# Optimization experiments

Measured on AMD Instinct MI355X. Metric: run time of the kernel, lower is better.

## Reference

```python
import jax, jax.numpy as jnp
import numpy as np
import math

NEG = -100000.0

def sliding_window_attention(q, k, v, window_size, padding_mask):
    # q,k,v: [B,H,L,D]; padding_mask: [B,L] (0 = pad)
    B, H, L, D = q.shape
    w = window_size // 2
    W = 2 * w + 1
    kp = jnp.pad(k, ((0, 0), (0, 0), (w, w), (0, 0)))
    vp = jnp.pad(v, ((0, 0), (0, 0), (w, w), (0, 0)))
    # window gather indices in padded coordinates: position i attends padded [i, i+2w]
    idx = jnp.arange(L)[:, None] + jnp.arange(W)[None, :]        # [L,W]
    pos = idx - w                                                 # true key positions
    valid = (pos >= 0) & (pos < L)                                # [L,W]
    k_win = kp[:, :, idx]                                         # [B,H,L,W,D]
    scores = jnp.einsum('bhld,bhlwd->bhlw', q, k_win)             # [B,H,L,W]
    scores = jnp.where(valid[None, None], scores, NEG)
    if padding_mask is not None:
        neigh_ok = padding_mask[:, jnp.clip(pos, 0, L - 1)]       # [B,L,W]
        scores = jnp.where(neigh_ok[:, None] == 0, NEG, scores)
    attn = jax.nn.softmax(scores / math.sqrt(D), axis=-1)         # [B,H,L,W]
    v_win = vp[:, :, idx]                                         # [B,H,L,W,D]
    values = jnp.einsum('bhlw,bhlwd->bhld', attn, v_win)
    return values

def setup_inputs() -> dict:
    key = jax.random.key(0)
    ks = jax.random.split(key, 5)
    B, L, input_dim, E, H = 2, 2048, 1024, 1024, 16
    x = jax.random.normal(ks[0], (B, L, input_dim), dtype=jnp.float32)
    padding_mask = jnp.ones((B, L), dtype=jnp.int32)
    # xavier-uniform linear weights (torch Linear stores [out, in])
    lim_qkv = math.sqrt(6.0 / (input_dim + 3 * E))
    W_qkv = jax.random.uniform(ks[1], (3 * E, input_dim), minval=-lim_qkv, maxval=lim_qkv, dtype=jnp.float32)
    b_qkv = jnp.zeros((3 * E,), dtype=jnp.float32)
    lim_o = math.sqrt(6.0 / (E + E))
    W_o = jax.random.uniform(ks[2], (E, E), minval=-lim_o, maxval=lim_o, dtype=jnp.float32)
    b_o = jnp.zeros((E,), dtype=jnp.float32)
    return {"x": x, "padding_mask": padding_mask, "W_qkv": W_qkv, "b_qkv": b_qkv, "W_o": W_o, "b_o": b_o}

def reference(x, padding_mask, W_qkv, b_qkv, W_o, b_o):
    B, L, _ = x.shape
    E = W_o.shape[0]
    H = 16
    hd = E // H
    window_size = 64
    qkv = x @ W_qkv.T + b_qkv                                  # [B,L,3E]
    qkv = qkv.reshape(B, L, H, 3 * hd).transpose(0, 2, 1, 3)   # [B,H,L,3hd]
    q, k, v = jnp.split(qkv, 3, axis=-1)
    values = sliding_window_attention(q, k, v, window_size, padding_mask)
    values = values.transpose(0, 2, 1, 3).reshape(B, L, E)
    o = values @ W_o.T + b_o
    return o
```

## Files before the change

### kernel.cpp

```cpp
#include <hip/hip_runtime.h>
#include <hip/hip_bf16.h>

typedef unsigned int u32;
typedef unsigned short u16;
typedef __attribute__((ext_vector_type(8))) short short8;
typedef __attribute__((ext_vector_type(4))) float f32x4;

#define NEG_SCORE (-100000.0f)

__device__ __forceinline__ float bflo(u32 u) { return __uint_as_float(u << 16); }
__device__ __forceinline__ float bfhi(u32 u) { return __uint_as_float(u & 0xffff0000u); }
__device__ __forceinline__ u16 f2bf(float f) {
    u32 u = __float_as_uint(f);
    u32 r = (u + 0x7fffu + ((u >> 16) & 1u)) >> 16;
    return (u16)r;
}

__device__ __forceinline__ void async16(const u16* g, u16* l) {
    __builtin_amdgcn_global_load_lds(
        (const __attribute__((address_space(1))) u32*)g,
        (__attribute__((address_space(3))) u32*)l,
        16, 0, 0);
}

__global__ __launch_bounds__(256) void f32_to_bf16_kernel(
    const float* __restrict__ src, u16* __restrict__ dst)
{
    const int i = blockIdx.x * 256 + threadIdx.x;
    const float4* s4 = (const float4*)src;
    float4 a = s4[2 * i + 0];
    float4 b = s4[2 * i + 1];
    uint4 o;
    o.x = (u32)f2bf(a.x) | ((u32)f2bf(a.y) << 16);
    o.y = (u32)f2bf(a.z) | ((u32)f2bf(a.w) << 16);
    o.z = (u32)f2bf(b.x) | ((u32)f2bf(b.y) << 16);
    o.w = (u32)f2bf(b.z) | ((u32)f2bf(b.w) << 16);
    ((uint4*)dst)[i] = o;
}

template <bool OUT_BF16>
__global__ __launch_bounds__(256) void gemm_bt_bias(
    const u16* __restrict__ A, const u16* __restrict__ Bt,
    const float* __restrict__ bias, void* __restrict__ Cv,
    int M, int N, int K)
{
    __shared__ u16 sA[128 * 32];
    __shared__ u16 sB[128 * 32];

    const int t    = threadIdx.x;
    const int m0   = blockIdx.y * 128;
    const int n0   = blockIdx.x * 128;
    const int lane = t & 63;
    const int wv   = t >> 6;
    const int wm   = (wv & 1) * 64;
    const int wn   = (wv >> 1) * 64;
    const int lr   = lane & 15;
    const int quad = lane >> 4;

    const u16* pa = A  + (size_t)(m0 + (t >> 2)) * K + ((t & 3) << 3);
    const u16* pb = Bt + (size_t)(n0 + (t >> 2)) * K + ((t & 3) << 3);
    u16* la = &sA[t * 8];
    u16* lb = &sB[t * 8];
    const size_t half = (size_t)64 * K;

    const f32x4 zero4 = {0.f, 0.f, 0.f, 0.f};
    f32x4 acc[4][4];
#pragma unroll
    for (int mt = 0; mt < 4; mt++)
#pragma unroll
        for (int nt = 0; nt < 4; nt++) acc[mt][nt] = zero4;

    for (int kk = 0; kk < K; kk += 32) {
        async16(pa + kk, la);
        async16(pa + kk + half, la + 2048);
        async16(pb + kk, lb);
        async16(pb + kk + half, lb + 2048);
        __syncthreads();

        short8 af[4], bfr[4];
#pragma unroll
        for (int mt = 0; mt < 4; mt++)
            af[mt] = *(const short8*)&sA[(wm + mt * 16 + lr) * 32 + quad * 8];
#pragma unroll
        for (int nt = 0; nt < 4; nt++)
            bfr[nt] = *(const short8*)&sB[(wn + nt * 16 + lr) * 32 + quad * 8];

#pragma unroll
        for (int mt = 0; mt < 4; mt++)
#pragma unroll
            for (int nt = 0; nt < 4; nt++)
                acc[mt][nt] = __builtin_amdgcn_mfma_f32_16x16x32_bf16(
                    af[mt], bfr[nt], acc[mt][nt], 0, 0, 0);
        __syncthreads();
    }

    float bv[4];
#pragma unroll
    for (int nt = 0; nt < 4; nt++)
        bv[nt] = bias[n0 + wn + nt * 16 + lr];

#pragma unroll
    for (int mt = 0; mt < 4; mt++) {
#pragma unroll
        for (int i = 0; i < 4; i++) {
            size_t row = (size_t)(m0 + wm + mt * 16 + quad * 4 + i);
#pragma unroll
            for (int nt = 0; nt < 4; nt++) {
                float v = acc[mt][nt][i] + bv[nt];
                size_t idx = row * N + n0 + wn + nt * 16 + lr;
                if (OUT_BF16) ((u16*)Cv)[idx] = f2bf(v);
                else          ((float*)Cv)[idx] = v;
            }
        }
    }
}

#define ATT_L 2048
#define ATT_C3 3072

__global__ __launch_bounds__(256) void swa_kernel(
    const u16* __restrict__ qkv, const int* __restrict__ mask,
    u16* __restrict__ values)
{
    __shared__ u16 sQ[4096];
    __shared__ u16 sK[8192];
    __shared__ u16 sP[8192];
    __shared__ u16 sV[9728];
    __shared__ int smask[128];
    __shared__ float sInv[64];

    const int t  = threadIdx.x;
    const int q0 = blockIdx.x * 64;
    const int h  = blockIdx.y;
    const int b  = blockIdx.z;
    const size_t base_bl = (size_t)b * ATT_L;
    const int* mrow = mask + b * ATT_L;
    const u16* hbase = qkv + base_bl * ATT_C3 + h * 192;

#pragma unroll
    for (int rep = 0; rep < 2; rep++) {
        int u = t + rep * 256;
        int r = u >> 3, j = u & 7;
        uint4 d = *(const uint4*)(hbase + (size_t)(q0 + r) * ATT_C3 + j * 8);
        *(uint4*)&sQ[(j >> 2) * 2048 + r * 32 + (j & 3) * 8] = d;
    }
#pragma unroll
    for (int rep = 0; rep < 4; rep++) {
        int u = t + rep * 256;
        int r = u >> 3, j = u & 7;
        int pos = q0 - 32 + r;
        int pc = min(max(pos, 0), ATT_L - 1);
        uint4 d = *(const uint4*)(hbase + (size_t)pc * ATT_C3 + 64 + j * 8);
        *(uint4*)&sK[(j >> 2) * 4096 + r * 32 + (j & 3) * 8] = d;
    }
#pragma unroll
    for (int rep = 0; rep < 4; rep++) {
        int u = t + rep * 256;
        int r = u >> 3, j = u & 7;
        int pos = q0 - 32 + r;
        uint4 d = make_uint4(0, 0, 0, 0);
        if (pos >= 0 && pos < ATT_L)
            d = *(const uint4*)(hbase + (size_t)pos * ATT_C3 + 128 + j * 8);
        *(uint2*)&sV[r * 76 + j * 8]     = make_uint2(d.x, d.y);
        *(uint2*)&sV[r * 76 + j * 8 + 4] = make_uint2(d.z, d.w);
    }
    if (t < 128) {
        int pos = q0 - 32 + t;
        smask[t] = (pos >= 0 && pos < ATT_L) ? mrow[pos] : 0;
    }
    __syncthreads();

    const int lane = t & 63;
    const int wv   = t >> 6;
    const int lr   = lane & 15;
    const int quad = lane >> 4;

    const int qm0 = wv * 16;
    short8 aq0 = *(const short8*)&sQ[0 * 2048 + (qm0 + lr) * 32 + quad * 8];
    short8 aq1 = *(const short8*)&sQ[1 * 2048 + (qm0 + lr) * 32 + quad * 8];

    const f32x4 zero4 = {0.f, 0.f, 0.f, 0.f};
    f32x4 acc[8];
#pragma unroll
    for (int nt = 0; nt < 8; nt++) {
        short8 b0 = *(const short8*)&sK[0 * 4096 + (nt * 16 + lr) * 32 + quad * 8];
        short8 b1 = *(const short8*)&sK[1 * 4096 + (nt * 16 + lr) * 32 + quad * 8];
        acc[nt] = __builtin_amdgcn_mfma_f32_16x16x32_bf16(aq0, b0, zero4, 0, 0, 0);
        acc[nt] = __builtin_amdgcn_mfma_f32_16x16x32_bf16(aq1, b1, acc[nt], 0, 0, 0);
    }

#pragma unroll
    for (int i = 0; i < 4; i++) {
        const int q_t = qm0 + quad * 4 + i;
        float sc[8];
#pragma unroll
        for (int nt = 0; nt < 8; nt++) {
            int nidx = nt * 16 + lr;
            int woff = nidx - q_t;
            float s;
            if ((unsigned)woff > 64u)       s = -1.0e30f;
            else if (smask[nidx] == 0)      s = NEG_SCORE * 0.125f;
            else                            s = acc[nt][i] * 0.125f;
            sc[nt] = s;
        }
        float mx = sc[0];
#pragma unroll
        for (int nt = 1; nt < 8; nt++) mx = fmaxf(mx, sc[nt]);
#pragma unroll
        for (int off = 1; off < 16; off <<= 1) mx = fmaxf(mx, __shfl_xor(mx, off));

        float den = 0.f;
#pragma unroll
        for (int nt = 0; nt < 8; nt++) {
            int nidx = nt * 16 + lr;
            u16 eb = f2bf(__expf(sc[nt] - mx));
            den += bflo((u32)eb);
            sP[(nidx >> 5) * 2048 + q_t * 32 + (nidx & 31)] = eb;
        }
#pragma unroll
        for (int off = 1; off < 16; off <<= 1) den += __shfl_xor(den, off);
        if (lr == 0) sInv[q_t] = 1.0f / den;
    }
    __syncthreads();

    const int dm0 = wv * 16;
    f32x4 acc2[4];
#pragma unroll
    for (int nt = 0; nt < 4; nt++) acc2[nt] = zero4;

#pragma unroll
    for (int c = 0; c < 4; c++) {
        short8 av;
#pragma unroll
        for (int j = 0; j < 8; j++)
            av[j] = (short)sV[(c * 32 + quad * 8 + j) * 76 + dm0 + lr];
#pragma unroll
        for (int nt = 0; nt < 4; nt++) {
            short8 bp = *(const short8*)&sP[c * 2048 + (nt * 16 + lr) * 32 + quad * 8];
            acc2[nt] = __builtin_amdgcn_mfma_f32_16x16x32_bf16(av, bp, acc2[nt], 0, 0, 0);
        }
    }

#pragma unroll
    for (int nt = 0; nt < 4; nt++) {
        int q_t = nt * 16 + lr;
        float iv = sInv[q_t];
        u32 w0 = (u32)f2bf(acc2[nt][0] * iv) | ((u32)f2bf(acc2[nt][1] * iv) << 16);
        u32 w1 = (u32)f2bf(acc2[nt][2] * iv) | ((u32)f2bf(acc2[nt][3] * iv) << 16);
        *(uint2*)&values[(base_bl + q0 + q_t) * 1024 + h * 64 + dm0 + quad * 4] =
            make_uint2(w0, w1);
    }
}

extern "C" void kernel_launch(void* const* d_in, const int* in_sizes, int n_in,
                              void* d_out, int out_size, void* d_ws, size_t ws_size,
                              hipStream_t stream) {
    const float* x     = (const float*)d_in[0];
    const int*   pmask = (const int*)d_in[1];
    const float* Wqkv  = (const float*)d_in[2];
    const float* bqkv  = (const float*)d_in[3];
    const float* Wo    = (const float*)d_in[4];
    const float* bo    = (const float*)d_in[5];
    float* out = (float*)d_out;

    u16* qkv    = (u16*)d_ws;
    u16* values = qkv    + (size_t)4096 * 3072;
    u16* xb     = values + (size_t)4096 * 1024;
    u16* Wqkvb  = xb     + (size_t)4096 * 1024;
    u16* Wob    = Wqkvb  + (size_t)3072 * 1024;

    f32_to_bf16_kernel<<<4096 * 1024 / (256 * 8), 256, 0, stream>>>(x, xb);
    f32_to_bf16_kernel<<<3072 * 1024 / (256 * 8), 256, 0, stream>>>(Wqkv, Wqkvb);
    f32_to_bf16_kernel<<<1024 * 1024 / (256 * 8), 256, 0, stream>>>(Wo, Wob);

    gemm_bt_bias<true><<<dim3(3072 / 128, 4096 / 128), 256, 0, stream>>>(
        xb, Wqkvb, bqkv, qkv, 4096, 3072, 1024);

    swa_kernel<<<dim3(2048 / 64, 16, 2), 256, 0, stream>>>(qkv, pmask, values);

    gemm_bt_bias<false><<<dim3(1024 / 128, 4096 / 128), 256, 0, stream>>>(
        values, Wob, bo, out, 4096, 1024, 1024);
}
```

Before: 174.7 us.

## Merge conversion launches, deepen GEMM K-step to 64, narrow output GEMM tile

Result: faster. 154.9 us (-11.3%).

```diff
diff --git a/kernel.cpp b/kernel.cpp
--- a/kernel.cpp
+++ b/kernel.cpp
@@ -23,10 +23,17 @@
         16, 0, 0);
 }
 
-__global__ __launch_bounds__(256) void f32_to_bf16_kernel(
-    const float* __restrict__ src, u16* __restrict__ dst)
+__global__ __launch_bounds__(256) void convert_all_kernel(
+    const float* __restrict__ x,    u16* __restrict__ xb,
+    const float* __restrict__ wqkv, u16* __restrict__ wqkvb,
+    const float* __restrict__ wo,   u16* __restrict__ wob)
 {
-    const int i = blockIdx.x * 256 + threadIdx.x;
+    const int bid = blockIdx.x;
+    const float* src; u16* dst; int base;
+    if (bid < 2048)      { src = x;    dst = xb;    base = bid; }
+    else if (bid < 3584) { src = wqkv; dst = wqkvb; base = bid - 2048; }
+    else                 { src = wo;   dst = wob;   base = bid - 3584; }
+    const int i = base * 256 + threadIdx.x;
     const float4* s4 = (const float4*)src;
     float4 a = s4[2 * i + 0];
     float4 b = s4[2 * i + 1];
@@ -38,65 +45,78 @@
     ((uint4*)dst)[i] = o;
 }
 
-template <bool OUT_BF16>
+template <int TN, bool OUT_BF16>
 __global__ __launch_bounds__(256) void gemm_bt_bias(
     const u16* __restrict__ A, const u16* __restrict__ Bt,
     const float* __restrict__ bias, void* __restrict__ Cv,
     int M, int N, int K)
 {
-    __shared__ u16 sA[128 * 32];
-    __shared__ u16 sB[128 * 32];
+    constexpr int NT = TN / 32;
+    __shared__ u16 sA[2 * 128 * 32];
+    __shared__ u16 sB[2 * TN * 32];
 
     const int t    = threadIdx.x;
     const int m0   = blockIdx.y * 128;
-    const int n0   = blockIdx.x * 128;
+    const int n0   = blockIdx.x * TN;
     const int lane = t & 63;
     const int wv   = t >> 6;
     const int wm   = (wv & 1) * 64;
-    const int wn   = (wv >> 1) * 64;
+    const int wn   = (wv >> 1) * (TN / 2);
     const int lr   = lane & 15;
     const int quad = lane >> 4;
 
-    const u16* pa = A  + (size_t)(m0 + (t >> 2)) * K + ((t & 3) << 3);
-    const u16* pb = Bt + (size_t)(n0 + (t >> 2)) * K + ((t & 3) << 3);
-    u16* la = &sA[t * 8];
-    u16* lb = &sB[t * 8];
-    const size_t half = (size_t)64 * K;
+    const int srow = t >> 2;
+    const int sj   = (t & 3) * 8;
 
     const f32x4 zero4 = {0.f, 0.f, 0.f, 0.f};
-    f32x4 acc[4][4];
+    f32x4 acc[4][NT];
 #pragma unroll
     for (int mt = 0; mt < 4; mt++)
 #pragma unroll
-        for (int nt = 0; nt < 4; nt++) acc[mt][nt] = zero4;
-
-    for (int kk = 0; kk < K; kk += 32) {
-        async16(pa + kk, la);
-        async16(pa + kk + half, la + 2048);
-        async16(pb + kk, lb);
-        async16(pb + kk + half, lb + 2048);
+        for (int nt = 0; nt < NT; nt++) acc[mt][nt] = zero4;
+
+    for (int kk = 0; kk < K; kk += 64) {
+#pragma unroll
+        for (int c = 0; c < 2; c++)
+#pragma unroll
+            for (int r2 = 0; r2 < 2; r2++) {
+                int row = srow + 64 * r2;
+                async16(A + (size_t)(m0 + row) * K + kk + c * 32 + sj,
+                        &sA[c * 4096 + row * 32 + sj]);
+            }
+#pragma unroll
+        for (int c = 0; c < 2; c++)
+#pragma unroll
+            for (int r2 = 0; r2 < TN / 64; r2++) {
+                int row = srow + 64 * r2;
+                async16(Bt + (size_t)(n0 + row) * K + kk + c * 32 + sj,
+                        &sB[c * (TN * 32) + row * 32 + sj]);
+            }
         __syncthreads();
 
-        short8 af[4], bfr[4];
-#pragma unroll
-        for (int mt = 0; mt < 4; mt++)
-            af[mt] = *(const short8*)&sA[(wm + mt * 16 + lr) * 32 + quad * 8];
-#pragma unroll
-        for (int nt = 0; nt < 4; nt++)
-            bfr[nt] = *(const short8*)&sB[(wn + nt * 16 + lr) * 32 + quad * 8];
-
-#pragma unroll
-        for (int mt = 0; mt < 4; mt++)
-#pragma unroll
-            for (int nt = 0; nt < 4; nt++)
-                acc[mt][nt] = __builtin_amdgcn_mfma_f32_16x16x32_bf16(
-                    af[mt], bfr[nt], acc[mt][nt], 0, 0, 0);
+#pragma unroll
+        for (int ks = 0; ks < 2; ks++) {
+            short8 af[4], bfr[NT];
+#pragma unroll
+            for (int mt = 0; mt < 4; mt++)
+                af[mt] = *(const short8*)&sA[ks * 4096 + (wm + mt * 16 + lr) * 32 + quad * 8];
+#pragma unroll
+            for (int nt = 0; nt < NT; nt++)
+                bfr[nt] = *(const short8*)&sB[ks * (TN * 32) + (wn + nt * 16 + lr) * 32 + quad * 8];
+
+#pragma unroll
+            for (int mt = 0; mt < 4; mt++)
+#pragma unroll
+                for (int nt = 0; nt < NT; nt++)
+                    acc[mt][nt] = __builtin_amdgcn_mfma_f32_16x16x32_bf16(
+                        af[mt], bfr[nt], acc[mt][nt], 0, 0, 0);
+        }
         __syncthreads();
     }
 
-    float bv[4];
-#pragma unroll
-    for (int nt = 0; nt < 4; nt++)
+    float bv[NT];
+#pragma unroll
+    for (int nt = 0; nt < NT; nt++)
         bv[nt] = bias[n0 + wn + nt * 16 + lr];
 
 #pragma unroll
@@ -105,7 +125,7 @@
         for (int i = 0; i < 4; i++) {
             size_t row = (size_t)(m0 + wm + mt * 16 + quad * 4 + i);
 #pragma unroll
-            for (int nt = 0; nt < 4; nt++) {
+            for (int nt = 0; nt < NT; nt++) {
                 float v = acc[mt][nt][i] + bv[nt];
                 size_t idx = row * N + n0 + wn + nt * 16 + lr;
                 if (OUT_BF16) ((u16*)Cv)[idx] = f2bf(v);
@@ -269,15 +289,13 @@
     u16* Wqkvb  = xb     + (size_t)4096 * 1024;
     u16* Wob    = Wqkvb  + (size_t)3072 * 1024;
 
-    f32_to_bf16_kernel<<<4096 * 1024 / (256 * 8), 256, 0, stream>>>(x, xb);
-    f32_to_bf16_kernel<<<3072 * 1024 / (256 * 8), 256, 0, stream>>>(Wqkv, Wqkvb);
-    f32_to_bf16_kernel<<<1024 * 1024 / (256 * 8), 256, 0, stream>>>(Wo, Wob);
-
-    gemm_bt_bias<true><<<dim3(3072 / 128, 4096 / 128), 256, 0, stream>>>(
+    convert_all_kernel<<<4096, 256, 0, stream>>>(x, xb, Wqkv, Wqkvb, Wo, Wob);
+
+    gemm_bt_bias<128, true><<<dim3(3072 / 128, 4096 / 128), 256, 0, stream>>>(
         xb, Wqkvb, bqkv, qkv, 4096, 3072, 1024);
 
     swa_kernel<<<dim3(2048 / 64, 16, 2), 256, 0, stream>>>(qkv, pmask, values);
 
-    gemm_bt_bias<false><<<dim3(1024 / 128, 4096 / 128), 256, 0, stream>>>(
+    gemm_bt_bias<64, false><<<dim3(1024 / 64, 4096 / 128), 256, 0, stream>>>(
         values, Wob, bo, out, 4096, 1024, 1024);
 }
```
